# Kernel tuning notes

Hardware: AMD Instinct MI355X
Metric: run time of the kernel (lower is better)

The kernel has to match this reference:

```python
import math
import jax, jax.numpy as jnp
import numpy as np

B, T, IN_DIM, DIM = 64, 3136, 147, 64
M = int(DIM * 0.5)  # random features
EPS = 1e-8


def _ln(x, g, b, eps=1e-5):
    mu = x.mean(-1, keepdims=True)
    var = ((x - mu) ** 2).mean(-1, keepdims=True)
    return (x - mu) / jnp.sqrt(var + eps) * g + b


def _prm_exp(x, w):
    # FAVOR+ positive random features: exp(w x - |x|^2/2) / sqrt(m)
    xd = 0.5 * (x * x).sum(-1, keepdims=True)          # (B,T,1)
    wtx = jnp.einsum('btd,md->btm', x, w)              # (B,T,M)
    return jnp.exp(wtx - xd) / math.sqrt(M)


def setup_inputs() -> dict:
    key = jax.random.key(0)
    ks = jax.random.split(key, 8)
    s = lambda k, shape: jax.random.normal(k, shape, jnp.float32) * 0.02
    x = jax.random.normal(ks[0], (B, T, IN_DIM), jnp.float32)
    # orthogonal random-feature matrix w (M, DIM), rows orthonormal, * sqrt(M)
    wr = np.random.default_rng(0).standard_normal((DIM, M)).astype(np.float32)
    q, _ = np.linalg.qr(wr)                            # (DIM, M) orthonormal cols
    w = jnp.asarray(q.T * math.sqrt(M))                # (M, DIM)
    return dict(
        x=x,
        W_proj1=s(ks[1], (IN_DIM, DIM)), b_proj1=jnp.zeros((DIM,), jnp.float32),
        W_kqv=s(ks[2], (DIM, 3 * DIM)), b_kqv=jnp.zeros((3 * DIM,), jnp.float32),
        W_proj2=s(ks[3], (DIM, DIM)), b_proj2=jnp.zeros((DIM,), jnp.float32),
        g1=jnp.ones((DIM,), jnp.float32), be1=jnp.zeros((DIM,), jnp.float32),
        g2=jnp.ones((DIM,), jnp.float32), be2=jnp.zeros((DIM,), jnp.float32),
        W_m1=s(ks[4], (DIM, DIM)), b_m1=jnp.zeros((DIM,), jnp.float32),
        W_m2=s(ks[5], (DIM, DIM)), b_m2=jnp.zeros((DIM,), jnp.float32),
        w=w,
    )


def reference(x, W_proj1, b_proj1, W_kqv, b_kqv, W_proj2, b_proj2,
              g1, be1, g2, be2, W_m1, b_m1, W_m2, b_m2, w):
    # project input tokens (in_dim -> dim)
    h = x @ W_proj1 + b_proj1                          # (B,T,DIM)
    # --- single_attn on ln1(h) ---
    hn = _ln(h, g1, be1)
    kqv = hn @ W_kqv + b_kqv
    k, q, v = jnp.split(kqv, 3, axis=-1)               # each (B,T,DIM)
    kp, qp = _prm_exp(k, w), _prm_exp(q, w)            # (B,T,M)
    D = jnp.einsum('btm,bm->bt', qp, kp.sum(1))[..., None]  # (B,T,1)
    kptv = jnp.einsum('btd,btm->bdm', v, kp)           # (B,DIM,M)
    y = jnp.einsum('btm,bdm->btd', qp, kptv) / (D + EPS)    # (B,T,DIM)
    y = v + (y @ W_proj2 + b_proj2)                    # v skip-connection
    # --- MLP block ---
    yn = _ln(y, g2, be2)
    m = jax.nn.gelu(yn @ W_m1 + b_m1, approximate=False) @ W_m2 + b_m2
    return y + m
```

## Files before the change

### kernel.cpp

```cpp
#include <hip/hip_runtime.h>


typedef __attribute__((ext_vector_type(8))) __bf16 bf16x8;
typedef __attribute__((ext_vector_type(4))) __bf16 bf16x4;
typedef __attribute__((ext_vector_type(4))) float  f32x4;

#define DEV __device__ __forceinline__

constexpr int Bc = 64, Tc = 3136, INDIM = 147, TM = 64;

constexpr size_t WS_QP   = 0;
constexpr size_t WS_ZERO = WS_QP + (size_t)Bc * Tc * 32 * 2;
constexpr size_t WS_KPS  = WS_ZERO;
constexpr size_t WS_KPTV = WS_KPS + (size_t)Bc * 32 * 4;
constexpr size_t WS_IMG  = WS_KPTV + (size_t)Bc * 64 * 32 * 4;
constexpr int ZCOUNT = Bc * 32 + Bc * 64 * 32;

constexpr int IMG_W1T   = 0;
constexpr int IMG_WKQVT = 10752;
constexpr int IMG_WF    = 24576;
constexpr int IMG_W2T   = 26880;
constexpr int IMG_WM1T  = 31488;
constexpr int IMG_WM2T  = 36096;

DEV f32x4 gemm_tile(const __bf16* A, int lda, const __bf16* Bm, int ldb,
                    int K, int r, int qd) {
    f32x4 acc = {0.f, 0.f, 0.f, 0.f};
    const __bf16* ap = A + r * lda + qd * 8;
    const __bf16* bp = Bm + r * ldb + qd * 8;
#pragma unroll
    for (int k = 0; k < 160; k += 32) {
        if (k >= K) break;
        bf16x8 av = *(const bf16x8*)(ap + k);
        bf16x8 bv = *(const bf16x8*)(bp + k);
        acc = __builtin_amdgcn_mfma_f32_16x16x32_bf16(av, bv, acc, 0, 0, 0);
    }
    return acc;
}

__global__ void prep_kernel(const float* __restrict__ W1, const float* __restrict__ Wkqv,
                            const float* __restrict__ wm, const float* __restrict__ W2,
                            const float* __restrict__ Wm1, const float* __restrict__ Wm2,
                            char* __restrict__ ws) {
    const int tid = blockIdx.x * blockDim.x + threadIdx.x;
    const int n = gridDim.x * blockDim.x;
    float* z = (float*)(ws + WS_ZERO);
    for (int i = tid; i < ZCOUNT; i += n) z[i] = 0.f;
    __bf16* img = (__bf16*)(ws + WS_IMG);
    for (int i = tid; i < 64 * 168; i += n) {
        int d = i / 168, k = i - d * 168;
        img[IMG_W1T + i] = (k < 147) ? (__bf16)W1[k * 64 + d] : (__bf16)0.f;
    }
    for (int i = tid; i < 192 * 72; i += n) {
        int c = i / 72, k = i - c * 72;
        img[IMG_WKQVT + i] = (k < 64) ? (__bf16)Wkqv[k * 192 + c] : (__bf16)0.f;
    }
    for (int i = tid; i < 32 * 72; i += n) {
        int m = i / 72, k = i - m * 72;
        img[IMG_WF + i] = (k < 64) ? (__bf16)wm[m * 64 + k] : (__bf16)0.f;
    }
    for (int i = tid; i < 64 * 72; i += n) {
        int c = i / 72, k = i - c * 72;
        img[IMG_W2T + i] = (k < 64) ? (__bf16)W2[k * 64 + c] : (__bf16)0.f;
    }
    for (int i = tid; i < 64 * 72; i += n) {
        int c = i / 72, k = i - c * 72;
        img[IMG_WM1T + i] = (k < 64) ? (__bf16)Wm1[k * 64 + c] : (__bf16)0.f;
    }
    for (int i = tid; i < 64 * 72; i += n) {
        int c = i / 72, k = i - c * 72;
        img[IMG_WM2T + i] = (k < 64) ? (__bf16)Wm2[k * 64 + c] : (__bf16)0.f;
    }
}

__global__ __launch_bounds__(512, 8) void pass1_kernel(
    const float* __restrict__ x, const float* __restrict__ b1,
    const float* __restrict__ bkqv, const float* __restrict__ g1,
    const float* __restrict__ be1, char* __restrict__ ws,
    float* __restrict__ vout) {
    __shared__ __align__(16) char smem[40576];
    __bf16* sXT  = (__bf16*)(smem);
    __bf16* sK   = (__bf16*)(smem);
    __bf16* sQ   = (__bf16*)(smem + 9216);
    __bf16* sH   = (__bf16*)(smem + 21504);
    __bf16* sKPT = (__bf16*)(smem + 21504);
    __bf16* sVT  = (__bf16*)(smem + 30720);
    float*  sXDK = (float*)(smem + 39936);
    float*  sXDQ = (float*)(smem + 40192);
    float*  sKPS = (float*)(smem + 40448);

    const int tid = threadIdx.x;
    const int wv = tid >> 6, lane = tid & 63, r = lane & 15, qd = lane >> 4;
    const int b = blockIdx.x & 63;
    const int t0 = (blockIdx.x >> 6) << 6;
    const __bf16* img = (const __bf16*)(ws + WS_IMG);

    {
        const float* xrow = x + (size_t)(b * Tc + t0) * INDIM;
        const f32x4* xp4 = (const f32x4*)xrow;
        for (int i4 = tid; i4 < 2352; i4 += 512) {
            f32x4 xv = xp4[i4];
            int g = i4 << 2;
            int t = g / 147;
            int k = g - t * 147;
#pragma unroll
            for (int j = 0; j < 4; j++) {
                sXT[t * 168 + k] = (__bf16)xv[j];
                k++;
                if (k == 147) { k = 0; t++; }
            }
        }
        for (int i = tid; i < TM * 21; i += 512) {
            int t = i / 21, k = 147 + (i - t * 21);
            sXT[t * 168 + k] = (__bf16)0.f;
        }
    }
    __syncthreads();

    for (int id = wv; id < 16; id += 8) {
        int m0 = (id & 3) * 16, n0 = (id >> 2) * 16;
        f32x4 acc = gemm_tile(sXT + m0 * 168, 168, img + IMG_W1T + n0 * 168, 168, 160, r, qd);
        int d = n0 + r;
        float bias = b1[d];
#pragma unroll
        for (int i = 0; i < 4; i++)
            sH[(m0 + qd * 4 + i) * 72 + d] = (__bf16)(acc[i] + bias);
    }
    __syncthreads();

    {
        int t = tid >> 3, p = tid & 7;
        __bf16* hp = sH + t * 72 + p * 8;
        bf16x8 hv = *(const bf16x8*)hp;
        float v[8], s1 = 0.f, s2 = 0.f;
#pragma unroll
        for (int i = 0; i < 8; i++) { v[i] = (float)hv[i]; s1 += v[i]; s2 += v[i] * v[i]; }
#pragma unroll
        for (int m = 1; m < 8; m <<= 1) { s1 += __shfl_xor(s1, m); s2 += __shfl_xor(s2, m); }
        float mu = s1 * (1.f / 64.f), var = s2 * (1.f / 64.f) - mu * mu;
        float rstd = rsqrtf(var + 1e-5f);
        bf16x8 o;
#pragma unroll
        for (int i = 0; i < 8; i++) {
            int d = p * 8 + i;
            o[i] = (__bf16)((v[i] - mu) * rstd * g1[d] + be1[d]);
        }
        *(bf16x8*)hp = o;
    }
    __syncthreads();

    for (int id = wv; id < 48; id += 8) {
        int which = id >> 4, tl = id & 15;
        int m0 = (tl & 3) * 16, n0 = (tl >> 2) * 16;
        const __bf16* Bm = img + IMG_WKQVT + which * 64 * 72 + n0 * 72;
        f32x4 acc = gemm_tile(sH + m0 * 72, 72, Bm, 72, 64, r, qd);
        int nn = n0 + r;
        float bias = bkqv[which * 64 + nn];
        if (which == 0) {
#pragma unroll
            for (int i = 0; i < 4; i++)
                sK[(m0 + qd * 4 + i) * 72 + nn] = (__bf16)(acc[i] + bias);
        } else if (which == 1) {
#pragma unroll
            for (int i = 0; i < 4; i++)
                sQ[(m0 + qd * 4 + i) * 72 + nn] = (__bf16)(acc[i] + bias);
        } else {
#pragma unroll
            for (int i = 0; i < 4; i++)
                sVT[nn * 72 + (m0 + qd * 4 + i)] = (__bf16)(acc[i] + bias);
        }
    }
    __syncthreads();

    {
        int t = tid >> 3, p = tid & 7;
        bf16x8 kv = *(const bf16x8*)(sK + t * 72 + p * 8);
        bf16x8 qv = *(const bf16x8*)(sQ + t * 72 + p * 8);
        float sk = 0.f, sq = 0.f;
#pragma unroll
        for (int i = 0; i < 8; i++) {
            float a = (float)kv[i]; sk += a * a;
            float c = (float)qv[i]; sq += c * c;
        }
#pragma unroll
        for (int m = 1; m < 8; m <<= 1) { sk += __shfl_xor(sk, m); sq += __shfl_xor(sq, m); }
        if (p == 0) { sXDK[t] = 0.5f * sk; sXDQ[t] = 0.5f * sq; }
        if (tid < 32) sKPS[tid] = 0.f;
        __bf16* vg = (__bf16*)(vout + (size_t)(b * Tc + t0) * 64);
        int dd = tid >> 3, tt0 = (tid & 7) * 8;
        *(bf16x8*)(vg + dd * 64 + tt0) = *(const bf16x8*)(sVT + dd * 72 + tt0);
    }
    __syncthreads();

    {
        const int wv4 = wv & 3;
        const bool isq = (wv >= 4);
        const __bf16* Aop = isq ? sQ : sK;
        const float* xd = isq ? sXDQ : sXDK;
        __bf16* qg = (__bf16*)(ws + WS_QP) + (size_t)(b * Tc + t0) * 32;
#pragma unroll
        for (int nb = 0; nb < 2; nb++) {
            int m0 = wv4 * 16, n0 = nb * 16;
            f32x4 acc = gemm_tile(Aop + m0 * 72, 72, img + IMG_WF + n0 * 72, 72, 64, r, qd);
            int m = n0 + r;
            if (!isq) {
                float loc = 0.f;
#pragma unroll
                for (int i = 0; i < 4; i++) {
                    int t = m0 + qd * 4 + i;
                    float val = __expf(acc[i] - xd[t]) * 0.17677669529663687f;
                    sKPT[m * 72 + t] = (__bf16)val;
                    loc += val;
                }
                loc += __shfl_xor(loc, 16);
                loc += __shfl_xor(loc, 32);
                if (qd == 0) atomicAdd(&sKPS[m], loc);
            } else {
#pragma unroll
                for (int i = 0; i < 4; i++) {
                    int t = m0 + qd * 4 + i;
                    float val = __expf(acc[i] - xd[t]) * 0.17677669529663687f;
                    qg[t * 32 + m] = (__bf16)val;
                }
            }
        }
    }
    __syncthreads();

    {
        float* kptv = (float*)(ws + WS_KPTV) + b * 2048;
        int mb = wv & 1, nb = wv >> 1;
        f32x4 acc = gemm_tile(sKPT + mb * 16 * 72, 72, sVT + nb * 16 * 72, 72, 64, r, qd);
#pragma unroll
        for (int i = 0; i < 4; i++) {
            int m = mb * 16 + qd * 4 + i, d = nb * 16 + r;
            atomicAdd(&kptv[d * 32 + m], acc[i]);
        }
        float* kps = (float*)(ws + WS_KPS) + b * 32;
        if (tid < 32) atomicAdd(&kps[tid], sKPS[tid]);
    }
}

__global__ __launch_bounds__(512, 8) void pass2_kernel(
    const float* __restrict__ b2, const float* __restrict__ g2,
    const float* __restrict__ be2, const float* __restrict__ bm1,
    const float* __restrict__ bm2, char* __restrict__ ws,
    float* __restrict__ out) {
    __shared__ __align__(16) char smem[38272];
    __bf16* sKPTV = (__bf16*)(smem);
    __bf16* sQPL  = (__bf16*)(smem + 5120);
    __bf16* sGL   = (__bf16*)(smem);
    __bf16* sVLT  = (__bf16*)(smem + 10240);
    __bf16* sYN   = (__bf16*)(smem + 10240);
    __bf16* sYA   = (__bf16*)(smem + 19456);
    __bf16* sYL   = (__bf16*)(smem + 28672);
    float*  sKPS  = (float*)(smem + 37888);
    float*  sDL   = (float*)(smem + 38016);

    const int tid = threadIdx.x;
    const int wv = tid >> 6, lane = tid & 63, r = lane & 15, qd = lane >> 4;
    const int b = blockIdx.x & 63;
    const int t0 = (blockIdx.x >> 6) << 6;
    const __bf16* img = (const __bf16*)(ws + WS_IMG);

    {
        const f32x4* kp4 = (const f32x4*)((const float*)(ws + WS_KPTV) + b * 2048);
        f32x4 kv = kp4[tid];
        int d = tid >> 3, m0 = (tid & 7) * 4;
        bf16x4 kb;
#pragma unroll
        for (int j = 0; j < 4; j++) kb[j] = (__bf16)kv[j];
        *(bf16x4*)(sKPTV + d * 40 + m0) = kb;
        if (tid < 32) sKPS[tid] = ((const float*)(ws + WS_KPS))[b * 32 + tid];
        if (tid < 256) {
            const bf16x8* qp8 = (const bf16x8*)((const __bf16*)(ws + WS_QP) +
                                                (size_t)(b * Tc + t0) * 32);
            bf16x8 q8 = qp8[tid];
            int t = tid >> 2, mm = (tid & 3) * 8;
            *(bf16x8*)(sQPL + t * 40 + mm) = q8;
        }
        const __bf16* vg = (const __bf16*)(out + (size_t)(b * Tc + t0) * 64);
        int dd = tid >> 3, tt0 = (tid & 7) * 8;
        *(bf16x8*)(sVLT + dd * 72 + tt0) = *(const bf16x8*)(vg + dd * 64 + tt0);
    }
    __syncthreads();

    {
        int t = tid >> 3, p = tid & 7;
        float s = 0.f;
#pragma unroll
        for (int j = 0; j < 4; j++) {
            int m = p * 4 + j;
            s += (float)sQPL[t * 40 + m] * sKPS[m];
        }
#pragma unroll
        for (int m = 1; m < 8; m <<= 1) s += __shfl_xor(s, m);
        if (p == 0) sDL[t] = s + 1e-8f;
    }
    __syncthreads();

    for (int id = wv; id < 16; id += 8) {
        int m0 = (id & 3) * 16, n0 = (id >> 2) * 16;
        f32x4 acc = gemm_tile(sQPL + m0 * 40, 40, sKPTV + n0 * 40, 40, 32, r, qd);
        int d = n0 + r;
#pragma unroll
        for (int i = 0; i < 4; i++) {
            int t = m0 + qd * 4 + i;
            sYA[t * 72 + d] = (__bf16)(acc[i] / sDL[t]);
        }
    }
    __syncthreads();

    for (int id = wv; id < 16; id += 8) {
        int m0 = (id & 3) * 16, n0 = (id >> 2) * 16;
        f32x4 acc = gemm_tile(sYA + m0 * 72, 72, img + IMG_W2T + n0 * 72, 72, 64, r, qd);
        int d = n0 + r;
        float bias = b2[d];
#pragma unroll
        for (int i = 0; i < 4; i++) {
            int t = m0 + qd * 4 + i;
            sYL[t * 72 + d] = (__bf16)(acc[i] + bias + (float)sVLT[d * 72 + t]);
        }
    }
    __syncthreads();

    {
        int t = tid >> 3, p = tid & 7;
        bf16x8 yv = *(const bf16x8*)(sYL + t * 72 + p * 8);
        float v[8], s1 = 0.f, s2 = 0.f;
#pragma unroll
        for (int i = 0; i < 8; i++) { v[i] = (float)yv[i]; s1 += v[i]; s2 += v[i] * v[i]; }
#pragma unroll
        for (int m = 1; m < 8; m <<= 1) { s1 += __shfl_xor(s1, m); s2 += __shfl_xor(s2, m); }
        float mu = s1 * (1.f / 64.f), var = s2 * (1.f / 64.f) - mu * mu;
        float rstd = rsqrtf(var + 1e-5f);
        bf16x8 o;
#pragma unroll
        for (int i = 0; i < 8; i++) {
            int d = p * 8 + i;
            o[i] = (__bf16)((v[i] - mu) * rstd * g2[d] + be2[d]);
        }
        *(bf16x8*)(sYN + t * 72 + p * 8) = o;
    }
    __syncthreads();

    for (int id = wv; id < 16; id += 8) {
        int m0 = (id & 3) * 16, n0 = (id >> 2) * 16;
        f32x4 acc = gemm_tile(sYN + m0 * 72, 72, img + IMG_WM1T + n0 * 72, 72, 64, r, qd);
        int d = n0 + r;
        float bias = bm1[d];
#pragma unroll
        for (int i = 0; i < 4; i++) {
            int t = m0 + qd * 4 + i;
            float z = acc[i] + bias;
            sGL[t * 72 + d] = (__bf16)(0.5f * z * (1.f + erff(z * 0.7071067811865475f)));
        }
    }
    __syncthreads();

    {
        float* og = out + (size_t)(b * Tc + t0) * 64;
        for (int id = wv; id < 16; id += 8) {
            int m0 = (id & 3) * 16, n0 = (id >> 2) * 16;
            f32x4 acc = gemm_tile(sGL + m0 * 72, 72, img + IMG_WM2T + n0 * 72, 72, 64, r, qd);
            int d = n0 + r;
            float bias = bm2[d];
#pragma unroll
            for (int i = 0; i < 4; i++) {
                int t = m0 + qd * 4 + i;
                og[t * 64 + d] = acc[i] + bias + (float)sYL[t * 72 + d];
            }
        }
    }
}

extern "C" void kernel_launch(void* const* d_in, const int* in_sizes, int n_in,
                              void* d_out, int out_size, void* d_ws, size_t ws_size,
                              hipStream_t stream) {
    (void)in_sizes; (void)n_in; (void)out_size; (void)ws_size;
    const float* x    = (const float*)d_in[0];
    const float* W1   = (const float*)d_in[1];
    const float* b1   = (const float*)d_in[2];
    const float* Wkqv = (const float*)d_in[3];
    const float* bkqv = (const float*)d_in[4];
    const float* W2   = (const float*)d_in[5];
    const float* b2   = (const float*)d_in[6];
    const float* g1   = (const float*)d_in[7];
    const float* be1  = (const float*)d_in[8];
    const float* g2   = (const float*)d_in[9];
    const float* be2  = (const float*)d_in[10];
    const float* Wm1  = (const float*)d_in[11];
    const float* bm1  = (const float*)d_in[12];
    const float* Wm2  = (const float*)d_in[13];
    const float* bm2  = (const float*)d_in[14];
    const float* wm   = (const float*)d_in[15];
    char* ws = (char*)d_ws;

    hipLaunchKernelGGL(prep_kernel, dim3(128), dim3(256), 0, stream,
                       W1, Wkqv, wm, W2, Wm1, Wm2, ws);
    hipLaunchKernelGGL(pass1_kernel, dim3(3136), dim3(512), 0, stream,
                       x, b1, bkqv, g1, be1, ws, (float*)d_out);
    hipLaunchKernelGGL(pass2_kernel, dim3(3136), dim3(512), 0, stream,
                       b2, g2, be2, bm1, bm2, ws, (float*)d_out);
}
```

Baseline: 315.5 us.

## Load x directly into MFMA fragments and fuse LayerNorm into proj1 epilogue

Each wave now reads its x rows straight from global memory into bf16 MFMA A-fragments, so the x tile is no longer staged through shared memory. Each wave computes a 16x32 output tile with two accumulators. LayerNorm statistics are reduced in registers via shuffles and combined across the two column halves through a small shared partial buffer, which removes one barrier and the separate LN pass. The cost is uncoalesced scalar global loads of x, since each lane reads 8 consecutive floats from a row with a 147-element stride.

```diff
diff --git a/kernel.cpp b/kernel.cpp
--- a/kernel.cpp
+++ b/kernel.cpp
@@ -37,6 +37,11 @@
     }
     return acc;
 }
+
+DEV f32x4 mfma16(bf16x8 a, bf16x8 b, f32x4 c) {
+    return __builtin_amdgcn_mfma_f32_16x16x32_bf16(a, b, c, 0, 0, 0);
+}
+DEV bf16x8 ld8(const __bf16* p) { return *(const bf16x8*)p; }
 
 __global__ void prep_kernel(const float* __restrict__ W1, const float* __restrict__ Wkqv,
                             const float* __restrict__ wm, const float* __restrict__ W2,
@@ -79,9 +84,9 @@
     const float* __restrict__ be1, char* __restrict__ ws,
     float* __restrict__ vout) {
     __shared__ __align__(16) char smem[40576];
-    __bf16* sXT  = (__bf16*)(smem);
     __bf16* sK   = (__bf16*)(smem);
     __bf16* sQ   = (__bf16*)(smem + 9216);
+    float*  sPart = (float*)(smem + 18432);
     __bf16* sH   = (__bf16*)(smem + 21504);
     __bf16* sKPT = (__bf16*)(smem + 21504);
     __bf16* sVT  = (__bf16*)(smem + 30720);
@@ -95,57 +100,80 @@
     const int t0 = (blockIdx.x >> 6) << 6;
     const __bf16* img = (const __bf16*)(ws + WS_IMG);
 
-    {
-        const float* xrow = x + (size_t)(b * Tc + t0) * INDIM;
-        const f32x4* xp4 = (const f32x4*)xrow;
-        for (int i4 = tid; i4 < 2352; i4 += 512) {
-            f32x4 xv = xp4[i4];
-            int g = i4 << 2;
-            int t = g / 147;
-            int k = g - t * 147;
-#pragma unroll
-            for (int j = 0; j < 4; j++) {
-                sXT[t * 168 + k] = (__bf16)xv[j];
-                k++;
-                if (k == 147) { k = 0; t++; }
+    const int tb = wv & 3;
+    const int nh = wv >> 2;
+    f32x4 acc0 = {0.f, 0.f, 0.f, 0.f}, acc1 = {0.f, 0.f, 0.f, 0.f};
+    {
+        const float* xr = x + (size_t)(b * Tc + t0 + tb * 16 + r) * INDIM;
+        bf16x8 af[5];
+#pragma unroll
+        for (int ks = 0; ks < 4; ks++) {
+            const float* p = xr + ks * 32 + qd * 8;
+            bf16x8 f;
+#pragma unroll
+            for (int j = 0; j < 8; j++) f[j] = (__bf16)p[j];
+            af[ks] = f;
+        }
+        {
+            const int c0 = 128 + qd * 8;
+            bf16x8 f;
+#pragma unroll
+            for (int j = 0; j < 8; j++) {
+                int c = c0 + j;
+                f[j] = (c < INDIM) ? (__bf16)xr[c] : (__bf16)0.f;
             }
-        }
-        for (int i = tid; i < TM * 21; i += 512) {
-            int t = i / 21, k = 147 + (i - t * 21);
-            sXT[t * 168 + k] = (__bf16)0.f;
-        }
-    }
-    __syncthreads();
-
-    for (int id = wv; id < 16; id += 8) {
-        int m0 = (id & 3) * 16, n0 = (id >> 2) * 16;
-        f32x4 acc = gemm_tile(sXT + m0 * 168, 168, img + IMG_W1T + n0 * 168, 168, 160, r, qd);
-        int d = n0 + r;
-        float bias = b1[d];
-#pragma unroll
-        for (int i = 0; i < 4; i++)
-            sH[(m0 + qd * 4 + i) * 72 + d] = (__bf16)(acc[i] + bias);
-    }
-    __syncthreads();
-
-    {
-        int t = tid >> 3, p = tid & 7;
-        __bf16* hp = sH + t * 72 + p * 8;
-        bf16x8 hv = *(const bf16x8*)hp;
-        float v[8], s1 = 0.f, s2 = 0.f;
-#pragma unroll
-        for (int i = 0; i < 8; i++) { v[i] = (float)hv[i]; s1 += v[i]; s2 += v[i] * v[i]; }
-#pragma unroll
-        for (int m = 1; m < 8; m <<= 1) { s1 += __shfl_xor(s1, m); s2 += __shfl_xor(s2, m); }
-        float mu = s1 * (1.f / 64.f), var = s2 * (1.f / 64.f) - mu * mu;
-        float rstd = rsqrtf(var + 1e-5f);
-        bf16x8 o;
-#pragma unroll
-        for (int i = 0; i < 8; i++) {
-            int d = p * 8 + i;
-            o[i] = (__bf16)((v[i] - mu) * rstd * g1[d] + be1[d]);
-        }
-        *(bf16x8*)hp = o;
+            af[4] = f;
+        }
+        const __bf16* bp0 = img + IMG_W1T + (nh * 32 + r) * 168 + qd * 8;
+        const __bf16* bp1 = bp0 + 16 * 168;
+#pragma unroll
+        for (int ks = 0; ks < 5; ks++) {
+            acc0 = mfma16(af[ks], ld8(bp0 + ks * 32), acc0);
+            acc1 = mfma16(af[ks], ld8(bp1 + ks * 32), acc1);
+        }
+    }
+    {
+        const int d0 = nh * 32 + r, d1 = d0 + 16;
+        const float b1a = b1[d0], b1b = b1[d1];
+        float p1[4], p2[4];
+#pragma unroll
+        for (int i = 0; i < 4; i++) {
+            acc0[i] += b1a; acc1[i] += b1b;
+            p1[i] = acc0[i] + acc1[i];
+            p2[i] = acc0[i] * acc0[i] + acc1[i] * acc1[i];
+        }
+#pragma unroll
+        for (int m = 1; m < 16; m <<= 1) {
+#pragma unroll
+            for (int i = 0; i < 4; i++) {
+                p1[i] += __shfl_xor(p1[i], m);
+                p2[i] += __shfl_xor(p2[i], m);
+            }
+        }
+        if (r == 0) {
+#pragma unroll
+            for (int i = 0; i < 4; i++) {
+                int t = tb * 16 + qd * 4 + i;
+                sPart[t * 4 + nh * 2 + 0] = p1[i];
+                sPart[t * 4 + nh * 2 + 1] = p2[i];
+            }
+        }
+    }
+    __syncthreads();
+    {
+        const int d0 = nh * 32 + r, d1 = d0 + 16;
+        const float g1a = g1[d0], g1b = g1[d1];
+        const float bea = be1[d0], beb = be1[d1];
+#pragma unroll
+        for (int i = 0; i < 4; i++) {
+            int t = tb * 16 + qd * 4 + i;
+            f32x4 pr = *(const f32x4*)(sPart + t * 4);
+            float s1 = pr[0] + pr[2], s2 = pr[1] + pr[3];
+            float mu = s1 * (1.f / 64.f), var = s2 * (1.f / 64.f) - mu * mu;
+            float rstd = rsqrtf(var + 1e-5f);
+            sH[t * 72 + d0] = (__bf16)((acc0[i] - mu) * rstd * g1a + bea);
+            sH[t * 72 + d1] = (__bf16)((acc1[i] - mu) * rstd * g1b + beb);
+        }
     }
     __syncthreads();
 
```

Measured after the change: 323.2 us. 2.4% more time.

## Fuse prep, pass1 and pass2 into one cooperative persistent kernel with grid syncs

Applied to the files above, without the earlier changes.

Replaces three separate kernel launches with one cooperative persistent kernel. Grid-wide barriers separate the weight-prep, reduction and output phases, and each block loops over tiles. The aim is to remove launch gaps and tail effects between the kernels. In exchange it adds grid-sync cost and a persistent-loop grid sized from occupancy, and it falls back to the old three-kernel path if the cooperative launch fails.

```diff
diff --git a/kernel.cpp b/kernel.cpp
--- a/kernel.cpp
+++ b/kernel.cpp
@@ -1,4 +1,7 @@
 #include <hip/hip_runtime.h>
+#include <hip/hip_cooperative_groups.h>
+
+namespace cg = cooperative_groups;
 
 
 typedef __attribute__((ext_vector_type(8))) __bf16 bf16x8;
@@ -8,6 +11,7 @@
 #define DEV __device__ __forceinline__
 
 constexpr int Bc = 64, Tc = 3136, INDIM = 147, TM = 64;
+constexpr int NTILE = 3136;
 
 constexpr size_t WS_QP   = 0;
 constexpr size_t WS_ZERO = WS_QP + (size_t)Bc * Tc * 32 * 2;
@@ -38,47 +42,44 @@
     return acc;
 }
 
-__global__ void prep_kernel(const float* __restrict__ W1, const float* __restrict__ Wkqv,
-                            const float* __restrict__ wm, const float* __restrict__ W2,
-                            const float* __restrict__ Wm1, const float* __restrict__ Wm2,
-                            char* __restrict__ ws) {
-    const int tid = blockIdx.x * blockDim.x + threadIdx.x;
-    const int n = gridDim.x * blockDim.x;
+
+DEV void prep_body(int gtid, int n,
+                   const float* W1, const float* Wkqv, const float* wm,
+                   const float* W2, const float* Wm1, const float* Wm2,
+                   char* ws) {
     float* z = (float*)(ws + WS_ZERO);
-    for (int i = tid; i < ZCOUNT; i += n) z[i] = 0.f;
-    __bf16* img = (__bf16*)(ws + WS_IMG);
-    for (int i = tid; i < 64 * 168; i += n) {
+    for (int i = gtid; i < ZCOUNT; i += n) z[i] = 0.f;
+    __bf16* wimg = (__bf16*)(ws + WS_IMG);
+    for (int i = gtid; i < 64 * 168; i += n) {
         int d = i / 168, k = i - d * 168;
-        img[IMG_W1T + i] = (k < 147) ? (__bf16)W1[k * 64 + d] : (__bf16)0.f;
-    }
-    for (int i = tid; i < 192 * 72; i += n) {
+        wimg[IMG_W1T + i] = (k < 147) ? (__bf16)W1[k * 64 + d] : (__bf16)0.f;
+    }
+    for (int i = gtid; i < 192 * 72; i += n) {
         int c = i / 72, k = i - c * 72;
-        img[IMG_WKQVT + i] = (k < 64) ? (__bf16)Wkqv[k * 192 + c] : (__bf16)0.f;
-    }
-    for (int i = tid; i < 32 * 72; i += n) {
+        wimg[IMG_WKQVT + i] = (k < 64) ? (__bf16)Wkqv[k * 192 + c] : (__bf16)0.f;
+    }
+    for (int i = gtid; i < 32 * 72; i += n) {
         int m = i / 72, k = i - m * 72;
-        img[IMG_WF + i] = (k < 64) ? (__bf16)wm[m * 64 + k] : (__bf16)0.f;
-    }
-    for (int i = tid; i < 64 * 72; i += n) {
+        wimg[IMG_WF + i] = (k < 64) ? (__bf16)wm[m * 64 + k] : (__bf16)0.f;
+    }
+    for (int i = gtid; i < 64 * 72; i += n) {
         int c = i / 72, k = i - c * 72;
-        img[IMG_W2T + i] = (k < 64) ? (__bf16)W2[k * 64 + c] : (__bf16)0.f;
-    }
-    for (int i = tid; i < 64 * 72; i += n) {
+        wimg[IMG_W2T + i] = (k < 64) ? (__bf16)W2[k * 64 + c] : (__bf16)0.f;
+    }
+    for (int i = gtid; i < 64 * 72; i += n) {
         int c = i / 72, k = i - c * 72;
-        img[IMG_WM1T + i] = (k < 64) ? (__bf16)Wm1[k * 64 + c] : (__bf16)0.f;
-    }
-    for (int i = tid; i < 64 * 72; i += n) {
+        wimg[IMG_WM1T + i] = (k < 64) ? (__bf16)Wm1[k * 64 + c] : (__bf16)0.f;
+    }
+    for (int i = gtid; i < 64 * 72; i += n) {
         int c = i / 72, k = i - c * 72;
-        img[IMG_WM2T + i] = (k < 64) ? (__bf16)Wm2[k * 64 + c] : (__bf16)0.f;
-    }
-}
-
-__global__ __launch_bounds__(512, 8) void pass1_kernel(
-    const float* __restrict__ x, const float* __restrict__ b1,
-    const float* __restrict__ bkqv, const float* __restrict__ g1,
-    const float* __restrict__ be1, char* __restrict__ ws,
-    float* __restrict__ vout) {
-    __shared__ __align__(16) char smem[40576];
+        wimg[IMG_WM2T + i] = (k < 64) ? (__bf16)Wm2[k * 64 + c] : (__bf16)0.f;
+    }
+}
+
+DEV void pass1_body(char* smem, int tid, int wv, int r, int qd, int b, int t0,
+                    const float* x, const float* b1, const float* bkqv,
+                    const float* g1, const float* be1, char* ws,
+                    float* vout) {
     __bf16* sXT  = (__bf16*)(smem);
     __bf16* sK   = (__bf16*)(smem);
     __bf16* sQ   = (__bf16*)(smem + 9216);
@@ -88,11 +89,6 @@
     float*  sXDK = (float*)(smem + 39936);
     float*  sXDQ = (float*)(smem + 40192);
     float*  sKPS = (float*)(smem + 40448);
-
-    const int tid = threadIdx.x;
-    const int wv = tid >> 6, lane = tid & 63, r = lane & 15, qd = lane >> 4;
-    const int b = blockIdx.x & 63;
-    const int t0 = (blockIdx.x >> 6) << 6;
     const __bf16* img = (const __bf16*)(ws + WS_IMG);
 
     {
@@ -241,12 +237,10 @@
     }
 }
 
-__global__ __launch_bounds__(512, 8) void pass2_kernel(
-    const float* __restrict__ b2, const float* __restrict__ g2,
-    const float* __restrict__ be2, const float* __restrict__ bm1,
-    const float* __restrict__ bm2, char* __restrict__ ws,
-    float* __restrict__ out) {
-    __shared__ __align__(16) char smem[38272];
+DEV void pass2_body(char* smem, int tid, int wv, int r, int qd, int b, int t0,
+                    const float* b2, const float* g2, const float* be2,
+                    const float* bm1, const float* bm2, char* ws,
+                    float* out) {
     __bf16* sKPTV = (__bf16*)(smem);
     __bf16* sQPL  = (__bf16*)(smem + 5120);
     __bf16* sGL   = (__bf16*)(smem);
@@ -256,11 +250,6 @@
     __bf16* sYL   = (__bf16*)(smem + 28672);
     float*  sKPS  = (float*)(smem + 37888);
     float*  sDL   = (float*)(smem + 38016);
-
-    const int tid = threadIdx.x;
-    const int wv = tid >> 6, lane = tid & 63, r = lane & 15, qd = lane >> 4;
-    const int b = blockIdx.x & 63;
-    const int t0 = (blockIdx.x >> 6) << 6;
     const __bf16* img = (const __bf16*)(ws + WS_IMG);
 
     {
@@ -372,6 +361,71 @@
             }
         }
     }
+}
+
+__global__ __launch_bounds__(512, 8) void fused_kernel(
+    const float* __restrict__ x,
+    const float* __restrict__ W1,  const float* __restrict__ b1,
+    const float* __restrict__ Wkqv, const float* __restrict__ bkqv,
+    const float* __restrict__ W2,  const float* __restrict__ b2,
+    const float* __restrict__ g1,  const float* __restrict__ be1,
+    const float* __restrict__ g2,  const float* __restrict__ be2,
+    const float* __restrict__ Wm1, const float* __restrict__ bm1,
+    const float* __restrict__ Wm2, const float* __restrict__ bm2,
+    const float* __restrict__ wm,
+    char* __restrict__ ws, float* __restrict__ out) {
+    __shared__ __align__(16) char smem[40576];
+    const int tid = threadIdx.x;
+    const int wv = tid >> 6, lane = tid & 63, r = lane & 15, qd = lane >> 4;
+
+    prep_body(blockIdx.x * 512 + tid, gridDim.x * 512,
+              W1, Wkqv, wm, W2, Wm1, Wm2, ws);
+    cg::this_grid().sync();
+
+    for (int tile = blockIdx.x; tile < NTILE; tile += gridDim.x) {
+        __syncthreads();
+        pass1_body(smem, tid, wv, r, qd, tile & 63, (tile >> 6) << 6,
+                   x, b1, bkqv, g1, be1, ws, out);
+    }
+    cg::this_grid().sync();
+
+    for (int tile = blockIdx.x; tile < NTILE; tile += gridDim.x) {
+        __syncthreads();
+        pass2_body(smem, tid, wv, r, qd, tile & 63, (tile >> 6) << 6,
+                   b2, g2, be2, bm1, bm2, ws, out);
+    }
+}
+
+__global__ void prep_kernel(const float* __restrict__ W1, const float* __restrict__ Wkqv,
+                            const float* __restrict__ wm, const float* __restrict__ W2,
+                            const float* __restrict__ Wm1, const float* __restrict__ Wm2,
+                            char* __restrict__ ws) {
+    prep_body(blockIdx.x * blockDim.x + threadIdx.x, gridDim.x * blockDim.x,
+              W1, Wkqv, wm, W2, Wm1, Wm2, ws);
+}
+
+__global__ __launch_bounds__(512, 8) void pass1_kernel(
+    const float* __restrict__ x, const float* __restrict__ b1,
+    const float* __restrict__ bkqv, const float* __restrict__ g1,
+    const float* __restrict__ be1, char* __restrict__ ws,
+    float* __restrict__ vout) {
+    __shared__ __align__(16) char smem[40576];
+    const int tid = threadIdx.x;
+    const int wv = tid >> 6, lane = tid & 63, r = lane & 15, qd = lane >> 4;
+    pass1_body(smem, tid, wv, r, qd, blockIdx.x & 63, (blockIdx.x >> 6) << 6,
+               x, b1, bkqv, g1, be1, ws, vout);
+}
+
+__global__ __launch_bounds__(512, 8) void pass2_kernel(
+    const float* __restrict__ b2, const float* __restrict__ g2,
+    const float* __restrict__ be2, const float* __restrict__ bm1,
+    const float* __restrict__ bm2, char* __restrict__ ws,
+    float* __restrict__ out) {
+    __shared__ __align__(16) char smem[38272];
+    const int tid = threadIdx.x;
+    const int wv = tid >> 6, lane = tid & 63, r = lane & 15, qd = lane >> 4;
+    pass2_body(smem, tid, wv, r, qd, blockIdx.x & 63, (blockIdx.x >> 6) << 6,
+               b2, g2, be2, bm1, bm2, ws, out);
 }
 
 extern "C" void kernel_launch(void* const* d_in, const int* in_sizes, int n_in,
@@ -395,11 +449,33 @@
     const float* bm2  = (const float*)d_in[14];
     const float* wm   = (const float*)d_in[15];
     char* ws = (char*)d_ws;
-
-    hipLaunchKernelGGL(prep_kernel, dim3(128), dim3(256), 0, stream,
-                       W1, Wkqv, wm, W2, Wm1, Wm2, ws);
-    hipLaunchKernelGGL(pass1_kernel, dim3(3136), dim3(512), 0, stream,
-                       x, b1, bkqv, g1, be1, ws, (float*)d_out);
-    hipLaunchKernelGGL(pass2_kernel, dim3(3136), dim3(512), 0, stream,
-                       b2, g2, be2, bm1, bm2, ws, (float*)d_out);
-}
+    float* outp = (float*)d_out;
+
+    static int coop_grid = 0;
+    if (coop_grid == 0) {
+        int maxb = 0;
+        if (hipOccupancyMaxActiveBlocksPerMultiprocessor(&maxb, fused_kernel, 512, 0)
+                != hipSuccess || maxb < 1)
+            maxb = 1;
+        long g = (long)maxb * 256;
+        if (g > NTILE) g = NTILE;
+        coop_grid = (int)g;
+    }
+
+    void* args[] = {(void*)&x, (void*)&W1, (void*)&b1, (void*)&Wkqv, (void*)&bkqv,
+                    (void*)&W2, (void*)&b2, (void*)&g1, (void*)&be1, (void*)&g2,
+                    (void*)&be2, (void*)&Wm1, (void*)&bm1, (void*)&Wm2, (void*)&bm2,
+                    (void*)&wm, (void*)&ws, (void*)&outp};
+    hipError_t e = hipLaunchCooperativeKernel((void*)fused_kernel,
+                                              dim3(coop_grid), dim3(512),
+                                              args, 0, stream);
+    if (e != hipSuccess) {
+        (void)hipGetLastError();
+        hipLaunchKernelGGL(prep_kernel, dim3(128), dim3(256), 0, stream,
+                           W1, Wkqv, wm, W2, Wm1, Wm2, ws);
+        hipLaunchKernelGGL(pass1_kernel, dim3(3136), dim3(512), 0, stream,
+                           x, b1, bkqv, g1, be1, ws, outp);
+        hipLaunchKernelGGL(pass2_kernel, dim3(3136), dim3(512), 0, stream,
+                           b2, g2, be2, bm1, bm2, ws, outp);
+    }
+}
```

New measurement: 522.3 us. 1.66x slower.
